# Kernel tuning notes

Measured on AMD Instinct MI355X. Metric: run time of the kernel, lower is better.

The kernel has to match this reference:

```python
import jax, jax.numpy as jnp
import numpy as np

NA = 50000   # nodes of type 'a'
NB = 50000   # nodes of type 'b'
E = 800000   # edges per cross relation
D = 256      # input feature dim == hidden_dim (SAGEConv lazy in-dim)
H = 256      # hidden_dim
EMB = 128    # embedding_dim
L = 2        # num_layer
# relation order in stacked weights: 0=(a,to,b), 1=(b,to,a), 2=(a,self_loop,a), 3=(b,self_loop,b)


def setup_inputs() -> dict:
    key = jax.random.key(0)
    ks = jax.random.split(key, 8)
    x_a = jax.random.normal(ks[0], (NA, D), jnp.float32)
    x_b = jax.random.normal(ks[1], (NB, D), jnp.float32)
    edge_ab = jax.random.randint(ks[2], (2, E), 0, NA, dtype=jnp.int32)  # row0: src in a, row1: dst in b
    edge_ba = jax.random.randint(ks[3], (2, E), 0, NB, dtype=jnp.int32)  # row0: src in b, row1: dst in a
    s = 1.0 / np.sqrt(H)
    Wl = jax.random.normal(ks[4], (L, 4, H, H), jnp.float32) * s  # lin_l weight (on aggregated neighbors)
    bl = jnp.zeros((L, 4, H), jnp.float32)                         # lin_l bias
    Wr = jax.random.normal(ks[5], (L, 4, H, H), jnp.float32) * s  # lin_r weight (root/self), no bias
    lin_W = jax.random.normal(ks[6], (H, EMB), jnp.float32) * s
    lin_b = jnp.zeros((EMB,), jnp.float32)
    return dict(x_a=x_a, x_b=x_b, edge_ab=edge_ab, edge_ba=edge_ba,
                Wl=Wl, bl=bl, Wr=Wr, lin_W=lin_W, lin_b=lin_b)


def _sage(x_src, x_dst, src, dst, n_dst, Wl, bl, Wr):
    # SAGEConv: mean-aggregate neighbor features, then lin_l(agg) + lin_r(x_dst)
    agg = jax.ops.segment_sum(x_src[src], dst, num_segments=n_dst)           # [n_dst, H]
    cnt = jax.ops.segment_sum(jnp.ones(src.shape, x_src.dtype), dst, num_segments=n_dst)
    mean = agg / jnp.maximum(cnt, 1.0)[:, None]                               # isolated dst -> 0
    return mean @ Wl + bl + x_dst @ Wr


def _sage_self(x, Wl, bl, Wr):
    # self-loop relation: each node has exactly one neighbor (itself), mean == x
    return x @ Wl + bl + x @ Wr


def reference(x_a, x_b, edge_ab, edge_ba, Wl, bl, Wr, lin_W, lin_b):
    xa, xb = x_a, x_b
    for l in range(L):
        new_a = (_sage(xb, xa, edge_ba[0], edge_ba[1], xa.shape[0], Wl[l, 1], bl[l, 1], Wr[l, 1])
                 + _sage_self(xa, Wl[l, 2], bl[l, 2], Wr[l, 2]))
        new_b = (_sage(xa, xb, edge_ab[0], edge_ab[1], xb.shape[0], Wl[l, 0], bl[l, 0], Wr[l, 0])
                 + _sage_self(xb, Wl[l, 3], bl[l, 3], Wr[l, 3]))
        xa, xb = jax.nn.relu(new_a), jax.nn.relu(new_b)
    return xa @ lin_W + lin_b, xb @ lin_W + lin_b
```

## Files before the change

### kernel.cpp

```cpp
#include <hip/hip_runtime.h>
#include <hip/hip_bf16.h>

#define NNA 50000
#define NNB 50000
#define NE  800000
#define HD  256
#define EMBD 128
#define NDST (NNA + NNB)

#define CONV_BLOCKS 2048
#define FILL_BLOCKS ((2 * NE) / 256)
#define PREP_IDS (2 * 2 * 512 * 256 + 1024 + 32768)
#define PREP_BLOCKS ((PREP_IDS + 255) / 256)

typedef __attribute__((ext_vector_type(4))) int            i32x4;
typedef __attribute__((ext_vector_type(4))) float          f32x4;
typedef __attribute__((ext_vector_type(8))) _Float16       f16x8;
typedef __attribute__((ext_vector_type(4))) unsigned short u16x4;
typedef __attribute__((ext_vector_type(8))) unsigned short u16x8;

static __device__ __forceinline__ float h2f(unsigned short u) {
  _Float16 h = __builtin_bit_cast(_Float16, u);
  return (float)h;
}
static __device__ __forceinline__ unsigned short f2h(float f) {
  _Float16 h = (_Float16)f;
  return __builtin_bit_cast(unsigned short, h);
}

static __device__ __forceinline__ void gload_lds16(const void* g, void* l) {
  __builtin_amdgcn_global_load_lds((const __attribute__((address_space(1))) void*)g,
                                   (__attribute__((address_space(3))) void*)l, 16, 0, 0);
}

__global__ __launch_bounds__(256)
void k_front(const float* __restrict__ xa, const float* __restrict__ xb,
             unsigned short* __restrict__ xout,
             const int* __restrict__ e_ba, const int* __restrict__ e_ab,
             int* __restrict__ cnt, unsigned short* __restrict__ slots,
             const float* __restrict__ Wl, const float* __restrict__ Wr,
             const float* __restrict__ bl, const float* __restrict__ linW,
             unsigned short* __restrict__ WcatT, float* __restrict__ bias,
             unsigned short* __restrict__ linWT) {
  int b = blockIdx.x;
  if (b < CONV_BLOCKS) {
    const int n4a = NNA * HD / 4;
    const int n4  = (NNA + NNB) * HD / 4;
    int i = b * 256 + threadIdx.x;
    const int stride = CONV_BLOCKS * 256;
    for (; i < n4; i += stride) {
      const float* src = (i < n4a) ? (xa + (size_t)i * 4) : (xb + (size_t)(i - n4a) * 4);
      f32x4 v = *reinterpret_cast<const f32x4*>(src);
      u16x4 o;
      o[0] = f2h(v[0]); o[1] = f2h(v[1]); o[2] = f2h(v[2]); o[3] = f2h(v[3]);
      reinterpret_cast<u16x4*>(xout)[i] = o;
    }
    return;
  }
  b -= CONV_BLOCKS;
  if (b < FILL_BLOCKS) {
    int e = b * 256 + threadIdx.x;
    int src, gdst;
    if (e < NE) {
      src = e_ba[e];
      gdst = e_ba[NE + e];
    } else {
      int f = e - NE;
      src = e_ab[f];
      gdst = NNA + e_ab[NE + f];
    }
    int pos = atomicAdd(&cnt[gdst], 1);
    if (pos < 64) slots[(size_t)gdst * 64 + pos] = (unsigned short)src;
    return;
  }
  b -= FILL_BLOCKS;
  {
    int id = b * 256 + threadIdx.x;
    if (id < 2 * 2 * 512 * 256) {
      int n = id & 255;
      int k = (id >> 8) & 511;
      int t = (id >> 17) & 1;
      int l = id >> 18;
      int rn = (t == 0) ? 1 : 0;
      int rs = (t == 0) ? 2 : 3;
      float v;
      if (k < HD) {
        v = Wl[((l * 4 + rn) * HD + k) * HD + n];
      } else {
        int kk = k - HD;
        v = Wr[((l * 4 + rn) * HD + kk) * HD + n]
          + Wl[((l * 4 + rs) * HD + kk) * HD + n]
          + Wr[((l * 4 + rs) * HD + kk) * HD + n];
      }
      WcatT[((l * 2 + t) * HD + n) * 512 + k] = f2h(v);
      return;
    }
    int id1 = id - 2 * 2 * 512 * 256;
    if (id1 < 2 * 2 * 256) {
      int n = id1 & 255; int t = (id1 >> 8) & 1; int l = id1 >> 9;
      int rn = (t == 0) ? 1 : 0;
      int rs = (t == 0) ? 2 : 3;
      bias[id1] = bl[(l * 4 + rn) * HD + n] + bl[(l * 4 + rs) * HD + n];
      return;
    }
    int id2 = id1 - 2 * 2 * 256;
    if (id2 < EMBD * HD) {
      int k = id2 & 255; int n = id2 >> 8;
      linWT[n * HD + k] = f2h(linW[k * EMBD + n]);
    }
  }
}

__global__ __launch_bounds__(256)
void k_aggregate(const unsigned short* __restrict__ xa,
                 const unsigned short* __restrict__ xb,
                 const unsigned short* __restrict__ slots,
                 const int* __restrict__ cnt,
                 unsigned short* __restrict__ mean_a, unsigned short* __restrict__ mean_b) {
  int w = blockIdx.x * 4 + (threadIdx.x >> 6);
  int lane = threadIdx.x & 63;
  const unsigned short* xsrc;
  unsigned short* outp;
  int deg = cnt[w];
  if (w < NNA) {
    xsrc = xb;
    outp = mean_a + (size_t)w * HD;
  } else {
    xsrc = xa;
    outp = mean_b + (size_t)(w - NNA) * HD;
  }
  int m = deg < 64 ? deg : 64;
  int s_all = (int)slots[(size_t)w * 64 + lane];
  const int half = lane >> 5;
  const int l31 = lane & 31;

  float acc[8];
#pragma unroll
  for (int k = 0; k < 8; ++k) acc[k] = 0.f;

  int j = 0;
  for (; j + 8 <= m; j += 8) {
    int sj[4];
#pragma unroll
    for (int i = 0; i < 4; ++i) sj[i] = __shfl(s_all, j + 2 * i + half);
    u16x8 v[4];
#pragma unroll
    for (int i = 0; i < 4; ++i)
      v[i] = *reinterpret_cast<const u16x8*>(xsrc + (size_t)sj[i] * HD + l31 * 8);
#pragma unroll
    for (int i = 0; i < 4; ++i)
#pragma unroll
      for (int k = 0; k < 8; ++k) acc[k] += h2f(v[i][k]);
  }
  for (; j + 2 <= m; j += 2) {
    int sj = __shfl(s_all, j + half);
    u16x8 v = *reinterpret_cast<const u16x8*>(xsrc + (size_t)sj * HD + l31 * 8);
#pragma unroll
    for (int k = 0; k < 8; ++k) acc[k] += h2f(v[k]);
  }
  if (j < m && half == 0) {
    int sj = __shfl(s_all, j);
    u16x8 v = *reinterpret_cast<const u16x8*>(xsrc + (size_t)sj * HD + l31 * 8);
#pragma unroll
    for (int k = 0; k < 8; ++k) acc[k] += h2f(v[k]);
  }

#pragma unroll
  for (int k = 0; k < 8; ++k) acc[k] += __shfl_xor(acc[k], 32);

  float inv = deg > 0 ? 1.0f / (float)deg : 0.0f;
  if (half == 0) {
    u16x8 o;
#pragma unroll
    for (int k = 0; k < 8; ++k) o[k] = f2h(acc[k] * inv);
    *reinterpret_cast<u16x8*>(outp + l31 * 8) = o;
  }
}

template <bool RELU, bool OUTF32>
__global__ __launch_bounds__(256)
void k_gemm(const unsigned short* __restrict__ Alo,
            const unsigned short* __restrict__ Ahi,
            const unsigned short* __restrict__ BT,
            const float* __restrict__ bias,
            void* __restrict__ Cout,
            int M, int N, int Ktot, int Klo,
            long long sA, long long sB, long long sBias, long long sCbytes) {
  const int z = blockIdx.z;
  Alo += (long long)z * sA;
  Ahi += (long long)z * sA;
  BT += (long long)z * sB;
  bias += (long long)z * sBias;
  Cout = (void*)((char*)Cout + (long long)z * sCbytes);

  __shared__ char smem[65536];
  const int t = threadIdx.x;
  const int bm = blockIdx.x, bn = blockIdx.y;
  const int lane = t & 63, wid = t >> 6;
  const int wm = wid >> 1, wn = wid & 1;
  const int l15 = lane & 15, l4 = lane >> 4;
  const int rgrp = lane >> 3;
  const int boff = (((lane & 7) ^ rgrp) << 4);

  f32x4 acc[4][4];
#pragma unroll
  for (int i = 0; i < 4; ++i)
#pragma unroll
    for (int j = 0; j < 4; ++j) acc[i][j] = (f32x4){0.f, 0.f, 0.f, 0.f};

  const int nks = Ktot >> 6;

  auto stage = [&](int ks, int buf) {
    const int kglob = ks << 6;
    const unsigned short* Asrc = (kglob < Klo) ? Alo : Ahi;
    const int kbase = (kglob < Klo) ? kglob : (kglob - Klo);
    char* sA_ = smem + buf * 16384;
    char* sB_ = smem + 32768 + buf * 16384;
#pragma unroll
    for (int i = 0; i < 4; ++i) {
      int rloc = wid * 32 + i * 8;
      int rA = bm * 128 + rloc + rgrp;
      if (rA >= M) rA = M - 1;
      const char* ga = (const char*)(Asrc + (size_t)rA * HD + kbase) + boff;
      gload_lds16(ga, sA_ + rloc * 128);
      int rB = bn * 128 + rloc + rgrp;
      const char* gb = (const char*)(BT + (size_t)rB * Ktot + kglob) + boff;
      gload_lds16(gb, sB_ + rloc * 128);
    }
  };

  stage(0, 0);
  __syncthreads();

  for (int ks = 0; ks < nks; ++ks) {
    if (ks + 1 < nks) stage(ks + 1, (ks + 1) & 1);
    const char* sA_ = smem + (ks & 1) * 16384;
    const char* sB_ = smem + 32768 + (ks & 1) * 16384;
#pragma unroll
    for (int kk = 0; kk < 2; ++kk) {
      f16x8 af[4], bfr[4];
#pragma unroll
      for (int f = 0; f < 4; ++f) {
        int r = wm * 64 + f * 16 + l15;
        af[f] = *reinterpret_cast<const f16x8*>(
            sA_ + r * 128 + ((kk * 64 + l4 * 16) ^ ((r & 7) << 4)));
        int n = wn * 64 + f * 16 + l15;
        bfr[f] = *reinterpret_cast<const f16x8*>(
            sB_ + n * 128 + ((kk * 64 + l4 * 16) ^ ((n & 7) << 4)));
      }
#pragma unroll
      for (int fm = 0; fm < 4; ++fm)
#pragma unroll
        for (int fn = 0; fn < 4; ++fn)
          acc[fm][fn] = __builtin_amdgcn_mfma_f32_16x16x32_f16(af[fm], bfr[fn], acc[fm][fn], 0, 0, 0);
    }
    __syncthreads();
  }

#pragma unroll
  for (int fm = 0; fm < 4; ++fm) {
    int row0 = bm * 128 + wm * 64 + fm * 16 + l4 * 4;
#pragma unroll
    for (int fn = 0; fn < 4; ++fn) {
      int col = bn * 128 + wn * 64 + fn * 16 + l15;
      float bv = bias[col];
      f32x4 d = acc[fm][fn];
#pragma unroll
      for (int r = 0; r < 4; ++r) {
        int rg = row0 + r;
        if (rg < M) {
          float v = d[r] + bv;
          if (RELU) v = v > 0.f ? v : 0.f;
          if (OUTF32)
            reinterpret_cast<float*>(Cout)[(size_t)rg * N + col] = v;
          else
            reinterpret_cast<unsigned short*>(Cout)[(size_t)rg * N + col] = f2h(v);
        }
      }
    }
  }
}


extern "C" void kernel_launch(void* const* d_in, const int* in_sizes, int n_in,
                              void* d_out, int out_size, void* d_ws, size_t ws_size,
                              hipStream_t stream) {
  const float* x_a  = (const float*)d_in[0];
  const float* x_b  = (const float*)d_in[1];
  const int*   e_ab = (const int*)d_in[2];
  const int*   e_ba = (const int*)d_in[3];
  const float* Wl   = (const float*)d_in[4];
  const float* bl   = (const float*)d_in[5];
  const float* Wr   = (const float*)d_in[6];
  const float* linW = (const float*)d_in[7];
  const float* linb = (const float*)d_in[8];
  float* out = (float*)d_out;

  char* ws = (char*)d_ws;
  size_t off = 0;
  auto alloc = [&](size_t bytes) {
    char* p = ws + off;
    off += (bytes + 255) & ~(size_t)255;
    return p;
  };
  unsigned short* x0   = (unsigned short*)alloc((size_t)2 * NNA * HD * 2);
  unsigned short* x1   = (unsigned short*)alloc((size_t)2 * NNA * HD * 2);
  unsigned short* mean = (unsigned short*)alloc((size_t)2 * NNA * HD * 2);
  int*            cnt  = (int*)alloc((size_t)NDST * 4);
  unsigned short* slots = (unsigned short*)alloc((size_t)NDST * 64 * 2);
  unsigned short* wcatT  = (unsigned short*)alloc((size_t)2 * 2 * 256 * 512 * 2);
  float*          biasv  = (float*)alloc((size_t)2 * 2 * 256 * 4);
  unsigned short* linWT  = (unsigned short*)alloc((size_t)EMBD * HD * 2);
  (void)ws_size; (void)in_sizes; (void)n_in; (void)out_size;

  hipMemsetAsync(cnt, 0, (size_t)NDST * 4, stream);

  k_front<<<CONV_BLOCKS + FILL_BLOCKS + PREP_BLOCKS, 256, 0, stream>>>(
      x_a, x_b, x0, e_ba, e_ab, cnt, slots, Wl, Wr, bl, linW, wcatT, biasv, linWT);

  unsigned short* xcur = x0;
  unsigned short* xnxt = x1;

  for (int l = 0; l < 2; ++l) {
    k_aggregate<<<(NNA + NNB) / 4, 256, 0, stream>>>(
        xcur, xcur + (size_t)NNA * HD, slots, cnt,
        mean, mean + (size_t)NNA * HD);
    dim3 g((NNA + 127) / 128, 2, 2);
    k_gemm<true, false><<<g, 256, 0, stream>>>(
        mean, xcur, wcatT + (size_t)l * 2 * 256 * 512, biasv + l * 2 * 256, xnxt,
        NNA, 256, 512, 256,
        (long long)NNA * HD, 256 * 512, 256, (long long)NNA * HD * 2);
    unsigned short* tmp = xcur; xcur = xnxt; xnxt = tmp;
  }

  dim3 gf((NNA + 127) / 128, 1, 2);
  k_gemm<false, true><<<gf, 256, 0, stream>>>(
      xcur, xcur, linWT, linb, out,
      NNA, EMBD, 256, 256,
      (long long)NNA * HD, 0, 0, (long long)NNA * EMBD * 4);
}
```

Baseline: 527.9 us.

## Switch to bf16, build deterministic sorted CSR, stop pre-summing self weights

```diff
diff --git a/kernel.cpp b/kernel.cpp
--- a/kernel.cpp
+++ b/kernel.cpp
@@ -8,24 +8,29 @@
 #define EMBD 128
 #define NDST (NNA + NNB)
 
+#define BSH 9
+#define NBK ((NDST + 511) >> 9)
+#define CAP 12288
+#define PART_CHUNK 4096
+#define PART_BLOCKS ((2 * NE + PART_CHUNK - 1) / PART_CHUNK)
+
 #define CONV_BLOCKS 2048
-#define FILL_BLOCKS ((2 * NE) / 256)
-#define PREP_IDS (2 * 2 * 512 * 256 + 1024 + 32768)
+#define KTOT 1024
+#define PREP_IDS (2 * 2 * KTOT * 256 + 1024 + 32768)
 #define PREP_BLOCKS ((PREP_IDS + 255) / 256)
 
 typedef __attribute__((ext_vector_type(4))) int            i32x4;
 typedef __attribute__((ext_vector_type(4))) float          f32x4;
-typedef __attribute__((ext_vector_type(8))) _Float16       f16x8;
+typedef __attribute__((ext_vector_type(8))) short          bf16x8;
 typedef __attribute__((ext_vector_type(4))) unsigned short u16x4;
 typedef __attribute__((ext_vector_type(8))) unsigned short u16x8;
 
-static __device__ __forceinline__ float h2f(unsigned short u) {
-  _Float16 h = __builtin_bit_cast(_Float16, u);
-  return (float)h;
-}
-static __device__ __forceinline__ unsigned short f2h(float f) {
-  _Float16 h = (_Float16)f;
-  return __builtin_bit_cast(unsigned short, h);
+static __device__ __forceinline__ float bf2f(unsigned short u) {
+  union { unsigned int i; float f; } v; v.i = ((unsigned int)u) << 16; return v.f;
+}
+static __device__ __forceinline__ unsigned short f2bf(float f) {
+  __hip_bfloat16 h = __float2bfloat16(f);
+  return *reinterpret_cast<unsigned short*>(&h);
 }
 
 static __device__ __forceinline__ void gload_lds16(const void* g, void* l) {
@@ -36,8 +41,6 @@
 __global__ __launch_bounds__(256)
 void k_front(const float* __restrict__ xa, const float* __restrict__ xb,
              unsigned short* __restrict__ xout,
-             const int* __restrict__ e_ba, const int* __restrict__ e_ab,
-             int* __restrict__ cnt, unsigned short* __restrict__ slots,
              const float* __restrict__ Wl, const float* __restrict__ Wr,
              const float* __restrict__ bl, const float* __restrict__ linW,
              unsigned short* __restrict__ WcatT, float* __restrict__ bias,
@@ -52,50 +55,32 @@
       const float* src = (i < n4a) ? (xa + (size_t)i * 4) : (xb + (size_t)(i - n4a) * 4);
       f32x4 v = *reinterpret_cast<const f32x4*>(src);
       u16x4 o;
-      o[0] = f2h(v[0]); o[1] = f2h(v[1]); o[2] = f2h(v[2]); o[3] = f2h(v[3]);
+      o[0] = f2bf(v[0]); o[1] = f2bf(v[1]); o[2] = f2bf(v[2]); o[3] = f2bf(v[3]);
       reinterpret_cast<u16x4*>(xout)[i] = o;
     }
     return;
   }
   b -= CONV_BLOCKS;
-  if (b < FILL_BLOCKS) {
-    int e = b * 256 + threadIdx.x;
-    int src, gdst;
-    if (e < NE) {
-      src = e_ba[e];
-      gdst = e_ba[NE + e];
-    } else {
-      int f = e - NE;
-      src = e_ab[f];
-      gdst = NNA + e_ab[NE + f];
-    }
-    int pos = atomicAdd(&cnt[gdst], 1);
-    if (pos < 64) slots[(size_t)gdst * 64 + pos] = (unsigned short)src;
-    return;
-  }
-  b -= FILL_BLOCKS;
   {
     int id = b * 256 + threadIdx.x;
-    if (id < 2 * 2 * 512 * 256) {
+    if (id < 2 * 2 * KTOT * 256) {
       int n = id & 255;
-      int k = (id >> 8) & 511;
-      int t = (id >> 17) & 1;
-      int l = id >> 18;
+      int k = (id >> 8) & (KTOT - 1);
+      int t = (id >> 18) & 1;
+      int l = id >> 19;
       int rn = (t == 0) ? 1 : 0;
       int rs = (t == 0) ? 2 : 3;
+      int seg = k >> 8;
+      int kk = k & 255;
       float v;
-      if (k < HD) {
-        v = Wl[((l * 4 + rn) * HD + k) * HD + n];
-      } else {
-        int kk = k - HD;
-        v = Wr[((l * 4 + rn) * HD + kk) * HD + n]
-          + Wl[((l * 4 + rs) * HD + kk) * HD + n]
-          + Wr[((l * 4 + rs) * HD + kk) * HD + n];
-      }
-      WcatT[((l * 2 + t) * HD + n) * 512 + k] = f2h(v);
+      if (seg == 0)      v = Wl[((l * 4 + rn) * HD + kk) * HD + n];
+      else if (seg == 1) v = Wr[((l * 4 + rn) * HD + kk) * HD + n];
+      else if (seg == 2) v = Wl[((l * 4 + rs) * HD + kk) * HD + n];
+      else               v = Wr[((l * 4 + rs) * HD + kk) * HD + n];
+      WcatT[((size_t)(l * 2 + t) * HD + n) * KTOT + k] = f2bf(v);
       return;
     }
-    int id1 = id - 2 * 2 * 512 * 256;
+    int id1 = id - 2 * 2 * KTOT * 256;
     if (id1 < 2 * 2 * 256) {
       int n = id1 & 255; int t = (id1 >> 8) & 1; int l = id1 >> 9;
       int rn = (t == 0) ? 1 : 0;
@@ -106,9 +91,109 @@
     int id2 = id1 - 2 * 2 * 256;
     if (id2 < EMBD * HD) {
       int k = id2 & 255; int n = id2 >> 8;
-      linWT[n * HD + k] = f2h(linW[k * EMBD + n]);
-    }
-  }
+      linWT[n * HD + k] = f2bf(linW[k * EMBD + n]);
+    }
+  }
+}
+
+__global__ __launch_bounds__(256)
+void k_part(const int* __restrict__ e_ba, const int* __restrict__ e_ab,
+            unsigned* __restrict__ tail, unsigned long long* __restrict__ csr_tmp) {
+  __shared__ unsigned bh[NBK];
+  __shared__ unsigned gbase[NBK];
+  __shared__ unsigned lpos[NBK];
+  const int tid = threadIdx.x;
+  const int ebase = blockIdx.x * PART_CHUNK;
+  int nvalid = 2 * NE - ebase;
+  if (nvalid > PART_CHUNK) nvalid = PART_CHUNK;
+
+  for (int i = tid; i < NBK; i += 256) { bh[i] = 0; lpos[i] = 0; }
+  __syncthreads();
+
+  unsigned sv[16], gv[16];
+#pragma unroll
+  for (int q = 0; q < 16; ++q) {
+    int i = q * 256 + tid;
+    int e = ebase + i;
+    unsigned s = 0, g = 0;
+    if (i < nvalid) {
+      if (e < NE) { s = (unsigned)e_ba[e]; g = (unsigned)e_ba[NE + e]; }
+      else { int f = e - NE; s = (unsigned)e_ab[f]; g = (unsigned)(NNA + e_ab[NE + f]); }
+      atomicAdd(&bh[g >> BSH], 1u);
+    }
+    sv[q] = s; gv[q] = g;
+  }
+  __syncthreads();
+
+  for (int i = tid; i < NBK; i += 256)
+    if (bh[i]) gbase[i] = atomicAdd(&tail[i], bh[i]);
+  __syncthreads();
+
+#pragma unroll
+  for (int q = 0; q < 16; ++q) {
+    int i = q * 256 + tid;
+    if (i < nvalid) {
+      unsigned g = gv[q];
+      unsigned bk = g >> BSH;
+      unsigned e = (unsigned)(ebase + i);
+      unsigned p = atomicAdd(&lpos[bk], 1u);
+      unsigned long long v = ((unsigned long long)(g & 511u) << 37)
+                           | ((unsigned long long)e << 16)
+                           | (unsigned long long)sv[q];
+      csr_tmp[(size_t)bk * CAP + gbase[bk] + p] = v;
+    }
+  }
+}
+
+__global__ __launch_bounds__(256)
+void k_bfill(const unsigned* __restrict__ tail, const unsigned long long* __restrict__ csr_tmp,
+             unsigned long long* __restrict__ slots64, int* __restrict__ cnt) {
+  const int b = blockIdx.x;
+  const int tid = threadIdx.x;
+  unsigned nb = tail[b];
+  if (nb > CAP) nb = CAP;
+  const int d0 = b << BSH;
+  const unsigned long long* src = csr_tmp + (size_t)b * CAP;
+
+  __shared__ unsigned lpos[512];
+  lpos[tid] = 0; lpos[tid + 256] = 0;
+  __syncthreads();
+
+  for (unsigned i = tid; i < nb; i += 256) {
+    unsigned long long v = src[i];
+    unsigned dl = (unsigned)(v >> 37);
+    unsigned p = atomicAdd(&lpos[dl], 1u);
+    if (p < 64) slots64[((size_t)(d0 + dl) << 6) + p] = v & 0x1FFFFFFFFFFULL;
+  }
+  __syncthreads();
+
+  int da = d0 + tid, db = d0 + tid + 256;
+  if (da < NDST) cnt[da] = (int)lpos[tid];
+  if (db < NDST) cnt[db] = (int)lpos[tid + 256];
+}
+
+__global__ __launch_bounds__(256)
+void k_sort(const unsigned long long* __restrict__ slots64, const int* __restrict__ cnt,
+            unsigned short* __restrict__ slots16) {
+  int w = blockIdx.x * 4 + (threadIdx.x >> 6);
+  int lane = threadIdx.x & 63;
+  int deg = cnt[w];
+  int m = deg < 64 ? deg : 64;
+  unsigned long long key = (lane < m) ? slots64[((size_t)w << 6) + lane] : ~0ULL;
+
+#pragma unroll
+  for (int k = 2; k <= 64; k <<= 1) {
+#pragma unroll
+    for (int j = k >> 1; j >= 1; j >>= 1) {
+      unsigned long long other = __shfl_xor(key, j);
+      bool up = ((lane & k) == 0);
+      bool lower = ((lane & j) == 0);
+      bool keep_min = (lower == up);
+      bool swap = keep_min ? (other < key) : (other > key);
+      if (swap) key = other;
+    }
+  }
+  slots16[((size_t)w << 6) + lane] = (unsigned short)(key & 0xFFFFULL);
 }
 
 __global__ __launch_bounds__(256)
@@ -150,19 +235,19 @@
 #pragma unroll
     for (int i = 0; i < 4; ++i)
 #pragma unroll
-      for (int k = 0; k < 8; ++k) acc[k] += h2f(v[i][k]);
+      for (int k = 0; k < 8; ++k) acc[k] += bf2f(v[i][k]);
   }
   for (; j + 2 <= m; j += 2) {
     int sj = __shfl(s_all, j + half);
     u16x8 v = *reinterpret_cast<const u16x8*>(xsrc + (size_t)sj * HD + l31 * 8);
 #pragma unroll
-    for (int k = 0; k < 8; ++k) acc[k] += h2f(v[k]);
+    for (int k = 0; k < 8; ++k) acc[k] += bf2f(v[k]);
   }
   if (j < m && half == 0) {
     int sj = __shfl(s_all, j);
     u16x8 v = *reinterpret_cast<const u16x8*>(xsrc + (size_t)sj * HD + l31 * 8);
 #pragma unroll
-    for (int k = 0; k < 8; ++k) acc[k] += h2f(v[k]);
+    for (int k = 0; k < 8; ++k) acc[k] += bf2f(v[k]);
   }
 
 #pragma unroll
@@ -172,7 +257,7 @@
   if (half == 0) {
     u16x8 o;
 #pragma unroll
-    for (int k = 0; k < 8; ++k) o[k] = f2h(acc[k] * inv);
+    for (int k = 0; k < 8; ++k) o[k] = f2bf(acc[k] * inv);
     *reinterpret_cast<u16x8*>(outp + l31 * 8) = o;
   }
 }
@@ -213,7 +298,7 @@
   auto stage = [&](int ks, int buf) {
     const int kglob = ks << 6;
     const unsigned short* Asrc = (kglob < Klo) ? Alo : Ahi;
-    const int kbase = (kglob < Klo) ? kglob : (kglob - Klo);
+    const int kbase = (kglob < Klo) ? kglob : (kglob & 255);
     char* sA_ = smem + buf * 16384;
     char* sB_ = smem + 32768 + buf * 16384;
 #pragma unroll
@@ -238,21 +323,21 @@
     const char* sB_ = smem + 32768 + (ks & 1) * 16384;
 #pragma unroll
     for (int kk = 0; kk < 2; ++kk) {
-      f16x8 af[4], bfr[4];
+      bf16x8 af[4], bfr[4];
 #pragma unroll
       for (int f = 0; f < 4; ++f) {
         int r = wm * 64 + f * 16 + l15;
-        af[f] = *reinterpret_cast<const f16x8*>(
+        af[f] = *reinterpret_cast<const bf16x8*>(
             sA_ + r * 128 + ((kk * 64 + l4 * 16) ^ ((r & 7) << 4)));
         int n = wn * 64 + f * 16 + l15;
-        bfr[f] = *reinterpret_cast<const f16x8*>(
+        bfr[f] = *reinterpret_cast<const bf16x8*>(
             sB_ + n * 128 + ((kk * 64 + l4 * 16) ^ ((n & 7) << 4)));
       }
 #pragma unroll
       for (int fm = 0; fm < 4; ++fm)
 #pragma unroll
         for (int fn = 0; fn < 4; ++fn)
-          acc[fm][fn] = __builtin_amdgcn_mfma_f32_16x16x32_f16(af[fm], bfr[fn], acc[fm][fn], 0, 0, 0);
+          acc[fm][fn] = __builtin_amdgcn_mfma_f32_16x16x32_bf16(af[fm], bfr[fn], acc[fm][fn], 0, 0, 0);
     }
     __syncthreads();
   }
@@ -274,7 +359,7 @@
           if (OUTF32)
             reinterpret_cast<float*>(Cout)[(size_t)rg * N + col] = v;
           else
-            reinterpret_cast<unsigned short*>(Cout)[(size_t)rg * N + col] = f2h(v);
+            reinterpret_cast<unsigned short*>(Cout)[(size_t)rg * N + col] = f2bf(v);
         }
       }
     }
@@ -307,29 +392,35 @@
   unsigned short* x1   = (unsigned short*)alloc((size_t)2 * NNA * HD * 2);
   unsigned short* mean = (unsigned short*)alloc((size_t)2 * NNA * HD * 2);
   int*            cnt  = (int*)alloc((size_t)NDST * 4);
-  unsigned short* slots = (unsigned short*)alloc((size_t)NDST * 64 * 2);
-  unsigned short* wcatT  = (unsigned short*)alloc((size_t)2 * 2 * 256 * 512 * 2);
+  unsigned long long* slots64 = (unsigned long long*)alloc((size_t)NDST * 64 * 8);
+  unsigned short* slots16 = (unsigned short*)alloc((size_t)NDST * 64 * 2);
+  unsigned*       tail = (unsigned*)alloc((size_t)NBK * 4);
+  unsigned long long* csr_tmp = (unsigned long long*)alloc((size_t)NBK * CAP * 8);
+  unsigned short* wcatT  = (unsigned short*)alloc((size_t)2 * 2 * 256 * KTOT * 2);
   float*          biasv  = (float*)alloc((size_t)2 * 2 * 256 * 4);
   unsigned short* linWT  = (unsigned short*)alloc((size_t)EMBD * HD * 2);
   (void)ws_size; (void)in_sizes; (void)n_in; (void)out_size;
 
-  hipMemsetAsync(cnt, 0, (size_t)NDST * 4, stream);
-
-  k_front<<<CONV_BLOCKS + FILL_BLOCKS + PREP_BLOCKS, 256, 0, stream>>>(
-      x_a, x_b, x0, e_ba, e_ab, cnt, slots, Wl, Wr, bl, linW, wcatT, biasv, linWT);
+  hipMemsetAsync(tail, 0, (size_t)NBK * 4, stream);
+
+  k_front<<<CONV_BLOCKS + PREP_BLOCKS, 256, 0, stream>>>(
+      x_a, x_b, x0, Wl, Wr, bl, linW, wcatT, biasv, linWT);
+  k_part<<<PART_BLOCKS, 256, 0, stream>>>(e_ba, e_ab, tail, csr_tmp);
+  k_bfill<<<NBK, 256, 0, stream>>>(tail, csr_tmp, slots64, cnt);
+  k_sort<<<NDST / 4, 256, 0, stream>>>(slots64, cnt, slots16);
 
   unsigned short* xcur = x0;
   unsigned short* xnxt = x1;
 
   for (int l = 0; l < 2; ++l) {
     k_aggregate<<<(NNA + NNB) / 4, 256, 0, stream>>>(
-        xcur, xcur + (size_t)NNA * HD, slots, cnt,
+        xcur, xcur + (size_t)NNA * HD, slots16, cnt,
         mean, mean + (size_t)NNA * HD);
     dim3 g((NNA + 127) / 128, 2, 2);
     k_gemm<true, false><<<g, 256, 0, stream>>>(
-        mean, xcur, wcatT + (size_t)l * 2 * 256 * 512, biasv + l * 2 * 256, xnxt,
-        NNA, 256, 512, 256,
-        (long long)NNA * HD, 256 * 512, 256, (long long)NNA * HD * 2);
+        mean, xcur, wcatT + (size_t)l * 2 * 256 * KTOT, biasv + l * 2 * 256, xnxt,
+        NNA, 256, KTOT, 256,
+        (long long)NNA * HD, (long long)256 * KTOT, 256, (long long)NNA * HD * 2);
     unsigned short* tmp = xcur; xcur = xnxt; xnxt = tmp;
   }
 
```

Result: no change. 537.4 us (+1.8%).
